# Optimization experiments

Measured on AMD Instinct MI355X. Metric: run time of the kernel, lower is better.

Reference implementation:

```python
import jax, jax.numpy as jnp
import numpy as np

B, S, D, H, HD = 1, 4096, 1024, 16, 64
HALF = HD // 2


def setup_inputs() -> dict:
    key = jax.random.key(0)
    ks = jax.random.split(key, 8)
    std = 0.02
    x = jax.random.normal(ks[0], (B, S, D), dtype=jnp.float32)
    wq_w = jax.random.normal(ks[1], (D, D), dtype=jnp.float32) * std
    wk_w = jax.random.normal(ks[2], (D, D), dtype=jnp.float32) * std
    wv_w = jax.random.normal(ks[3], (D, D), dtype=jnp.float32) * std
    wo_w = jax.random.normal(ks[4], (D, D), dtype=jnp.float32) * std
    wq_b = jnp.zeros((D,), jnp.float32)
    wk_b = jnp.zeros((D,), jnp.float32)
    wv_b = jnp.zeros((D,), jnp.float32)
    wo_b = jnp.zeros((D,), jnp.float32)
    # LLaMA-style rotary frequencies: theta = 10000^{-2i/HD}
    inv_freq = 1.0 / (10000.0 ** (jnp.arange(0, HD, 2, dtype=jnp.float32) / HD))  # [HALF]
    t = jnp.arange(S, dtype=jnp.float32)
    angles = jnp.outer(t, inv_freq)  # [S, HALF]
    freqs_cos = jnp.cos(angles)
    freqs_sin = jnp.sin(angles)
    # causal additive mask (finite large-negative to stay grad-safe)
    mask = jnp.triu(jnp.full((S, S), -1e9, dtype=jnp.float32), k=1)[None, None]
    return {
        "x": x, "start_pos": 0, "freqs_cos": freqs_cos, "freqs_sin": freqs_sin,
        "mask": mask,
        "wq_w": wq_w, "wq_b": wq_b, "wk_w": wk_w, "wk_b": wk_b,
        "wv_w": wv_w, "wv_b": wv_b, "wo_w": wo_w, "wo_b": wo_b,
    }


def _apply_rope(t, cos, sin):
    # t: [B, S, H, HD]; cos/sin: [S, HALF]. Complex multiply on consecutive pairs.
    b, s, h, hd = t.shape
    t2 = t.reshape(b, s, h, hd // 2, 2)
    x0, x1 = t2[..., 0], t2[..., 1]
    c = cos[None, :, None, :]
    sn = sin[None, :, None, :]
    o0 = x0 * c - x1 * sn
    o1 = x0 * sn + x1 * c
    return jnp.stack([o0, o1], axis=-1).reshape(b, s, h, hd)


def reference(x, start_pos, freqs_cos, freqs_sin, mask,
              wq_w, wq_b, wk_w, wk_b, wv_w, wv_b, wo_w, wo_b):
    bsz, seqlen, dim = x.shape
    q = (x @ wq_w.T + wq_b).reshape(bsz, seqlen, H, HD)
    k = (x @ wk_w.T + wk_b).reshape(bsz, seqlen, H, HD)
    v = (x @ wv_w.T + wv_b).reshape(bsz, seqlen, H, HD)
    q = _apply_rope(q, freqs_cos, freqs_sin)
    k = _apply_rope(k, freqs_cos, freqs_sin)
    # [B, H, S, HD]
    q = q.transpose(0, 2, 1, 3)
    k = k.transpose(0, 2, 1, 3)
    v = v.transpose(0, 2, 1, 3)
    scores = jnp.einsum('bhqd,bhkd->bhqk', q, k) / jnp.sqrt(jnp.float32(HD))
    scores = scores + mask
    probs = jax.nn.softmax(scores.astype(jnp.float32), axis=-1).astype(q.dtype)
    out = jnp.einsum('bhqk,bhkd->bhqd', probs, v)  # [B, H, S, HD]
    out = out.transpose(0, 2, 1, 3).reshape(bsz, seqlen, dim)
    return out @ wo_w.T + wo_b
```

## Files before the change

kernel.cpp:

```cpp
#include <hip/hip_runtime.h>


#define S_LEN 4096
#define DIM   1024
#define NH    16
#define HD    64

typedef __attribute__((ext_vector_type(8))) short bf16x8;
typedef __attribute__((ext_vector_type(4))) float f32x4;

__device__ __forceinline__ unsigned short f2b(float f) {
  union { float f; unsigned int u; } v; v.f = f;
  unsigned int r = (v.u + 0x7fffu + ((v.u >> 16) & 1u)) >> 16;
  return (unsigned short)r;
}
__device__ __forceinline__ float b2f(unsigned short h) {
  union { unsigned int u; float f; } v; v.u = ((unsigned int)h) << 16;
  return v.f;
}
__device__ __forceinline__ unsigned int pk2t(float a, float b) {
  union { float f; unsigned int u; } x, y; x.f = a; y.f = b;
  return (x.u >> 16) | (y.u & 0xffff0000u);
}
__device__ __forceinline__ void gload16(const void* g, void* l) {
  __builtin_amdgcn_global_load_lds(
      (const __attribute__((address_space(1))) unsigned int*)g,
      (__attribute__((address_space(3))) unsigned int*)l, 16, 0, 0);
}
__device__ __forceinline__ f32x4 fzero4() { f32x4 z = {0.f, 0.f, 0.f, 0.f}; return z; }

__global__ void cvt_all(const float* __restrict__ x, const float* __restrict__ wq,
                        const float* __restrict__ wk, const float* __restrict__ wv,
                        const float* __restrict__ wo, const float* __restrict__ qb,
                        const float* __restrict__ kb, const float* __restrict__ vbs,
                        const float* __restrict__ ob, unsigned short* __restrict__ xb,
                        unsigned short* __restrict__ wqkvb, unsigned short* __restrict__ wobb,
                        float* __restrict__ biasq, float* __restrict__ biaso) {
  int i = blockIdx.x * 256 + threadIdx.x;
  if (i < 2097152) {
    const float* src; unsigned short* dst; int off;
    if (i < 1048576)      { src = x;  dst = xb;              off = i; }
    else if (i < 1310720) { src = wq; dst = wqkvb;           off = i - 1048576; }
    else if (i < 1572864) { src = wk; dst = wqkvb + 1048576; off = i - 1310720; }
    else if (i < 1835008) { src = wv; dst = wqkvb + 2097152; off = i - 1572864; }
    else                  { src = wo; dst = wobb;            off = i - 1835008; }
    float4 v = ((const float4*)src)[off];
    unsigned int lo = (unsigned int)f2b(v.x) | ((unsigned int)f2b(v.y) << 16);
    unsigned int hi = (unsigned int)f2b(v.z) | ((unsigned int)f2b(v.w) << 16);
    ((uint2*)dst)[off] = make_uint2(lo, hi);
  } else if (i < 2097152 + 1024) {
    int j = i - 2097152;
    if (j < 256)      ((float4*)biasq)[j]              = ((const float4*)qb)[j];
    else if (j < 512) ((float4*)(biasq + 1024))[j-256] = ((const float4*)kb)[j-256];
    else if (j < 768) ((float4*)(biasq + 2048))[j-512] = ((const float4*)vbs)[j-512];
    else              ((float4*)biaso)[j-768]          = ((const float4*)ob)[j-768];
  }
}

__global__ __launch_bounds__(256) void gemm_qkv(
    const unsigned short* __restrict__ A, const unsigned short* __restrict__ B,
    const float* __restrict__ bias, unsigned short* __restrict__ dq,
    unsigned short* __restrict__ dk, unsigned short* __restrict__ vtout,
    const float* __restrict__ fc, const float* __restrict__ fs, int K) {
  __shared__ alignas(16) unsigned short sA[2][128 * 32];
  __shared__ alignas(16) unsigned short sB[2][128 * 32];
  const int tid = threadIdx.x;
  const int lane = tid & 63, wave = tid >> 6;
  const int ln = lane & 15, quad = lane >> 4;
  const int bm = blockIdx.x * 128, bn = blockIdx.y * 128;
  const int wr = (wave >> 1) * 64, wc = (wave & 1) * 64;

  f32x4 acc[4][4];
#pragma unroll
  for (int i = 0; i < 4; ++i)
#pragma unroll
    for (int j = 0; j < 4; ++j) acc[i][j] = fzero4();

#pragma unroll
  for (int i = 0; i < 2; ++i) {
    int o = (i * 256 + tid) * 16;
    int e = o >> 1;
    int row = e >> 5, col = e & 31;
    gload16(A + (size_t)(bm + row) * K + col, (char*)sA[0] + o);
    gload16(B + (size_t)(bn + row) * K + col, (char*)sB[0] + o);
  }

  int buf = 0;
  for (int k0 = 0; k0 < K; k0 += 32, buf ^= 1) {
    __syncthreads();
    if (k0 + 32 < K) {
#pragma unroll
      for (int i = 0; i < 2; ++i) {
        int o = (i * 256 + tid) * 16;
        int e = o >> 1;
        int row = e >> 5, col = e & 31;
        gload16(A + (size_t)(bm + row) * K + k0 + 32 + col, (char*)sA[buf ^ 1] + o);
        gload16(B + (size_t)(bn + row) * K + k0 + 32 + col, (char*)sB[buf ^ 1] + o);
      }
    }
    bf16x8 af[4], bfr[4];
#pragma unroll
    for (int i = 0; i < 4; ++i) {
      af[i]  = *(const bf16x8*)&sA[buf][(wr + i * 16 + ln) * 32 + quad * 8];
      bfr[i] = *(const bf16x8*)&sB[buf][(wc + i * 16 + ln) * 32 + quad * 8];
    }
#pragma unroll
    for (int i = 0; i < 4; ++i)
#pragma unroll
      for (int j = 0; j < 4; ++j)
        acc[i][j] = __builtin_amdgcn_mfma_f32_16x16x32_bf16(af[i], bfr[j], acc[i][j], 0, 0, 0);
  }

  const int bufi = bn >> 10;
  const int hq = ((bn & 1023) + wc) >> 6;
  if (bufi < 2) {
    unsigned short* const base = bufi == 0 ? dq : dk;
    const float qsc = bufi == 0 ? 0.180336880f : 1.0f;
#pragma unroll
    for (int i = 0; i < 4; ++i)
#pragma unroll
      for (int j = 0; j < 4; ++j) {
        int n = bn + wc + j * 16 + ln;
        float bi = bias[n];
        int hd = j * 16 + ln;
        int pi = hd >> 1;
        bool evn = (ln & 1) == 0;
#pragma unroll
        for (int r = 0; r < 4; ++r) {
          int m = bm + wr + i * 16 + quad * 4 + r;
          float val = acc[i][j][r] + bi;
          float par = __shfl_xor(val, 1);
          float c = fc[m * 32 + pi], sn = fs[m * 32 + pi];
          float o = evn ? (val * c - par * sn) : (par * sn + val * c);
          base[((size_t)(hq * S_LEN + m)) * HD + hd] = f2b(o * qsc);
        }
      }
  } else {
    __syncthreads();
    unsigned short* scr =
        (wave < 2 ? (unsigned short*)sA : (unsigned short*)sB) + (wave & 1) * 4096;
#pragma unroll
    for (int i = 0; i < 4; ++i)
#pragma unroll
      for (int j = 0; j < 4; ++j) {
        int n = bn + wc + j * 16 + ln;
        float bi = bias[n];
        int hd = j * 16 + ln;
#pragma unroll
        for (int r = 0; r < 4; ++r) {
          int sl = i * 16 + quad * 4 + r;
          int byte = hd * 128 + ((((sl >> 3) ^ (hd & 7)) << 4)) + (sl & 7) * 2;
          *(unsigned short*)((char*)scr + byte) = f2b(acc[i][j][r] + bi);
        }
      }
#pragma unroll
    for (int pass = 0; pass < 4; ++pass) {
      int row = pass * 16 + ln;
      uint4 d0 = *(uint4*)((char*)scr + row * 128 + (((quad * 2) ^ (row & 7)) << 4));
      uint4 d1 = *(uint4*)((char*)scr + row * 128 + (((quad * 2 + 1) ^ (row & 7)) << 4));
      uint4* dst = (uint4*)(vtout + ((size_t)(hq * HD + row)) * S_LEN + bm + wr + quad * 16);
      dst[0] = d0;
      dst[1] = d1;
    }
  }
}

__global__ __launch_bounds__(256) void gemm_out(
    const unsigned short* __restrict__ A, const unsigned short* __restrict__ B,
    const float* __restrict__ bias, float* __restrict__ outF, int N, int K) {
  __shared__ alignas(16) unsigned short sA[2][128 * 32];
  __shared__ alignas(16) unsigned short sB[2][64 * 32];
  const int tid = threadIdx.x;
  const int lane = tid & 63, wave = tid >> 6;
  const int ln = lane & 15, quad = lane >> 4;
  const int bm = blockIdx.x * 128, bn = blockIdx.y * 64;
  const int wr = (wave >> 1) * 64, wc = (wave & 1) * 32;

  f32x4 acc[4][2];
#pragma unroll
  for (int i = 0; i < 4; ++i)
#pragma unroll
    for (int j = 0; j < 2; ++j) acc[i][j] = fzero4();

  {
#pragma unroll
    for (int i = 0; i < 2; ++i) {
      int o = (i * 256 + tid) * 16;
      int e = o >> 1;
      int row = e >> 5, col = e & 31;
      gload16(A + (size_t)(bm + row) * K + col, (char*)sA[0] + o);
    }
    int o = tid * 16;
    int e = o >> 1;
    int row = e >> 5, col = e & 31;
    gload16(B + (size_t)(bn + row) * K + col, (char*)sB[0] + o);
  }

  int buf = 0;
  for (int k0 = 0; k0 < K; k0 += 32, buf ^= 1) {
    __syncthreads();
    if (k0 + 32 < K) {
#pragma unroll
      for (int i = 0; i < 2; ++i) {
        int o = (i * 256 + tid) * 16;
        int e = o >> 1;
        int row = e >> 5, col = e & 31;
        gload16(A + (size_t)(bm + row) * K + k0 + 32 + col, (char*)sA[buf ^ 1] + o);
      }
      int o = tid * 16;
      int e = o >> 1;
      int row = e >> 5, col = e & 31;
      gload16(B + (size_t)(bn + row) * K + k0 + 32 + col, (char*)sB[buf ^ 1] + o);
    }
    bf16x8 af[4], bfr[2];
#pragma unroll
    for (int i = 0; i < 4; ++i)
      af[i] = *(const bf16x8*)&sA[buf][(wr + i * 16 + ln) * 32 + quad * 8];
#pragma unroll
    for (int j = 0; j < 2; ++j)
      bfr[j] = *(const bf16x8*)&sB[buf][(wc + j * 16 + ln) * 32 + quad * 8];
#pragma unroll
    for (int i = 0; i < 4; ++i)
#pragma unroll
      for (int j = 0; j < 2; ++j)
        acc[i][j] = __builtin_amdgcn_mfma_f32_16x16x32_bf16(af[i], bfr[j], acc[i][j], 0, 0, 0);
  }

#pragma unroll
  for (int i = 0; i < 4; ++i)
#pragma unroll
    for (int j = 0; j < 2; ++j) {
      int n = bn + wc + j * 16 + ln;
      float bi = bias[n];
#pragma unroll
      for (int r = 0; r < 4; ++r) {
        int m = bm + wr + i * 16 + quad * 4 + r;
        outF[(size_t)m * N + n] = acc[i][j][r] + bi;
      }
    }
}

__device__ __forceinline__ bf16x8 lds_swz(const unsigned short* s, int row, int chunk) {
  int byte = row * 128 + ((chunk ^ (row & 7)) << 4);
  return *(const bf16x8*)((const char*)s + byte);
}

__global__ __launch_bounds__(512, 4) void flash_kernel(
    const unsigned short* __restrict__ qg, const unsigned short* __restrict__ kg,
    const unsigned short* __restrict__ vtg, unsigned short* __restrict__ attn) {
  __shared__ alignas(16) unsigned short sK[2][2][64 * 64];
  __shared__ alignas(16) unsigned short sV[2][2][64 * 64];

  const int tid = threadIdx.x;
  const int lane = tid & 63, wave = tid >> 6;
  const int w = wave & 3, grp = wave >> 2;
  const int ln = lane & 15, quad = lane >> 4;
  const int c = blockIdx.x;
  const int h = c & 15;
  const int qt = 63 - (c >> 4);
  const int qrow = qt * 64 + w * 16;

  const unsigned short* qh = qg + (size_t)h * (S_LEN * HD);
  const unsigned short* kh = kg + (size_t)h * (S_LEN * HD);
  const unsigned short* vh = vtg + (size_t)h * (HD * S_LEN);

  bf16x8 qf[2];
  qf[0] = *(const bf16x8*)(qh + (size_t)(qrow + ln) * HD + quad * 8);
  qf[1] = *(const bf16x8*)(qh + (size_t)(qrow + ln) * HD + 32 + quad * 8);

  f32x4 o_acc[4];
  f32x4 l_acc = fzero4();
#pragma unroll
  for (int t = 0; t < 4; ++t) o_acc[t] = fzero4();
  bf16x8 ones;
#pragma unroll
  for (int j = 0; j < 8; ++j) ones[j] = (short)0x3F80;

  const int nst = (qt + 2) >> 1;
  const int srow = tid >> 3, sch = tid & 7;
  const int kswz = (sch ^ (srow & 7)) << 3;

  gload16(kh + (size_t)srow * HD + kswz, (char*)sK[0][0] + tid * 16);
  gload16(kh + (size_t)(64 + srow) * HD + kswz, (char*)sK[0][1] + tid * 16);
  gload16(vh + (size_t)srow * S_LEN + kswz, (char*)sV[0][0] + tid * 16);
  gload16(vh + (size_t)srow * S_LEN + 64 + kswz, (char*)sV[0][1] + tid * 16);

  int buf = 0;
  for (int s = 0; s < nst; ++s, buf ^= 1) {
    __syncthreads();
    if (s + 1 < nst) {
      const int kvE = (2 * s + 2) * 64, kvO = kvE + 64;
      gload16(kh + (size_t)(kvE + srow) * HD + kswz, (char*)sK[buf ^ 1][0] + tid * 16);
      gload16(kh + (size_t)(kvO + srow) * HD + kswz, (char*)sK[buf ^ 1][1] + tid * 16);
      gload16(vh + (size_t)srow * S_LEN + kvE + kswz, (char*)sV[buf ^ 1][0] + tid * 16);
      gload16(vh + (size_t)srow * S_LEN + kvO + kswz, (char*)sV[buf ^ 1][1] + tid * 16);
    }
    const int kt = 2 * s + grp;
    if (kt > qt) continue;
    const int kv0 = kt * 64;
    const unsigned short* kp = sK[buf][grp];
    const unsigned short* vp = sV[buf][grp];

    f32x4 sc[4];
#pragma unroll
    for (int t = 0; t < 4; ++t) sc[t] = fzero4();
#pragma unroll
    for (int t = 0; t < 4; ++t) {
      bf16x8 kb0 = lds_swz(kp, t * 16 + ln, quad);
      bf16x8 kb1 = lds_swz(kp, t * 16 + ln, 4 + quad);
      sc[t] = __builtin_amdgcn_mfma_f32_16x16x32_bf16(kb0, qf[0], sc[t], 0, 0, 0);
      sc[t] = __builtin_amdgcn_mfma_f32_16x16x32_bf16(kb1, qf[1], sc[t], 0, 0, 0);
    }

    float e[4][4];
    if (kt == qt) {
#pragma unroll
      for (int t = 0; t < 4; ++t)
#pragma unroll
        for (int r = 0; r < 4; ++r) {
          int kvl = 16 * t + quad * 4 + r;
          e[t][r] = (kvl <= w * 16 + ln) ? __builtin_amdgcn_exp2f(sc[t][r]) : 0.0f;
        }
    } else {
#pragma unroll
      for (int t = 0; t < 4; ++t)
#pragma unroll
        for (int r = 0; r < 4; ++r) e[t][r] = __builtin_amdgcn_exp2f(sc[t][r]);
    }

    unsigned int x0 = pk2t(e[0][0], e[0][1]), x1 = pk2t(e[0][2], e[0][3]);
    unsigned int y0 = pk2t(e[1][0], e[1][1]), y1 = pk2t(e[1][2], e[1][3]);
    unsigned int z0 = pk2t(e[2][0], e[2][1]), z1 = pk2t(e[2][2], e[2][3]);
    unsigned int w0 = pk2t(e[3][0], e[3][1]), w1 = pk2t(e[3][2], e[3][3]);
    auto a32 = __builtin_amdgcn_permlane32_swap(x0, y0, false, false);
    auto a16 = __builtin_amdgcn_permlane16_swap(a32[0], a32[1], false, false);
    auto b32 = __builtin_amdgcn_permlane32_swap(x1, y1, false, false);
    auto b16 = __builtin_amdgcn_permlane16_swap(b32[0], b32[1], false, false);
    auto c32 = __builtin_amdgcn_permlane32_swap(z0, w0, false, false);
    auto c16 = __builtin_amdgcn_permlane16_swap(c32[0], c32[1], false, false);
    auto d32 = __builtin_amdgcn_permlane32_swap(z1, w1, false, false);
    auto d16 = __builtin_amdgcn_permlane16_swap(d32[0], d32[1], false, false);
    union { uint4 u; bf16x8 b; } pa0u, pa1u;
    pa0u.u = make_uint4(a16[0], b16[0], a16[1], b16[1]);
    pa1u.u = make_uint4(c16[0], d16[0], c16[1], d16[1]);
    const bf16x8 pa0 = pa0u.b, pa1 = pa1u.b;

    l_acc = __builtin_amdgcn_mfma_f32_16x16x32_bf16(pa0, ones, l_acc, 0, 0, 0);
    l_acc = __builtin_amdgcn_mfma_f32_16x16x32_bf16(pa1, ones, l_acc, 0, 0, 0);

#pragma unroll
    for (int t = 0; t < 4; ++t) {
      bf16x8 vb0 = lds_swz(vp, t * 16 + ln, quad);
      bf16x8 vb1 = lds_swz(vp, t * 16 + ln, 4 + quad);
      o_acc[t] = __builtin_amdgcn_mfma_f32_16x16x32_bf16(pa0, vb0, o_acc[t], 0, 0, 0);
      o_acc[t] = __builtin_amdgcn_mfma_f32_16x16x32_bf16(pa1, vb1, o_acc[t], 0, 0, 0);
    }
  }

  __syncthreads();
  float* mrg = (float*)sK;
  const int mi = (w * 64 + lane) * 20;
  if (grp == 1) {
    *(f32x4*)&mrg[mi +  0] = o_acc[0];
    *(f32x4*)&mrg[mi +  4] = o_acc[1];
    *(f32x4*)&mrg[mi +  8] = o_acc[2];
    *(f32x4*)&mrg[mi + 12] = o_acc[3];
    *(f32x4*)&mrg[mi + 16] = l_acc;
  }
  __syncthreads();
  if (grp == 0) {
    o_acc[0] += *(const f32x4*)&mrg[mi + 0];
    o_acc[1] += *(const f32x4*)&mrg[mi + 4];
    o_acc[2] += *(const f32x4*)&mrg[mi + 8];
    o_acc[3] += *(const f32x4*)&mrg[mi + 12];
    l_acc += *(const f32x4*)&mrg[mi + 16];
    float inv[4];
#pragma unroll
    for (int r = 0; r < 4; ++r) inv[r] = 1.0f / l_acc[r];
#pragma unroll
    for (int t = 0; t < 4; ++t)
#pragma unroll
      for (int r = 0; r < 4; ++r) {
        int row = qrow + quad * 4 + r;
        attn[(size_t)row * DIM + h * HD + t * 16 + ln] = f2b(o_acc[t][r] * inv[r]);
      }
  }
}

extern "C" void kernel_launch(void* const* d_in, const int* in_sizes, int n_in,
                              void* d_out, int out_size, void* d_ws, size_t ws_size,
                              hipStream_t stream) {
  const float* x    = (const float*)d_in[0];
  const float* fc   = (const float*)d_in[2];
  const float* fs   = (const float*)d_in[3];
  const float* wqw  = (const float*)d_in[5];
  const float* wqb  = (const float*)d_in[6];
  const float* wkw  = (const float*)d_in[7];
  const float* wkb  = (const float*)d_in[8];
  const float* wvw  = (const float*)d_in[9];
  const float* wvb  = (const float*)d_in[10];
  const float* wow  = (const float*)d_in[11];
  const float* wobf = (const float*)d_in[12];
  float* out = (float*)d_out;

  char* ws = (char*)d_ws;
  const size_t MB = (size_t)1 << 20;
  unsigned short* xb    = (unsigned short*)(ws + 0);
  unsigned short* wqkvb = (unsigned short*)(ws + 8 * MB);
  unsigned short* wobb  = (unsigned short*)(ws + 16 * MB);
  float* biasq = (float*)(ws + 18 * MB);
  float* biaso = (float*)(ws + 18 * MB + 65536);
  unsigned short* qb_ = (unsigned short*)(ws + 19 * MB);
  unsigned short* kb_ = (unsigned short*)(ws + 27 * MB);
  unsigned short* vt  = (unsigned short*)(ws + 35 * MB);
  unsigned short* attn = (unsigned short*)(ws + 0);

  cvt_all<<<8196, 256, 0, stream>>>(x, wqw, wkw, wvw, wow, wqb, wkb, wvb, wobf,
                                    xb, wqkvb, wobb, biasq, biaso);
  gemm_qkv<<<dim3(32, 24), 256, 0, stream>>>(xb, wqkvb, biasq, qb_, kb_, vt, fc, fs, 1024);
  flash_kernel<<<1024, 512, 0, stream>>>(qb_, kb_, vt, attn);
  gemm_out<<<dim3(32, 16), 256, 0, stream>>>(attn, wobb, biaso, out, 1024, 1024);
}
```

Baseline: 249.8 us.

## Enlarge QKV GEMM tiles to 256x256x64 with swizzled LDS and 512 threads

Reworks the QKV projection GEMM so each block computes a 256x256 output tile with 8 waves and a K-step of 64. LDS staging now uses an XOR swizzle to avoid bank conflicts, and the V-transpose epilogue is adapted to the wider tiles. The aim is more data reuse per LDS load and fewer global loads per output. In exchange the grid shrinks to 192 blocks, which may underfill the 256 CUs, and the larger accumulators raise register and LDS pressure (128KB of LDS).

```diff
diff --git a/kernel.cpp b/kernel.cpp
--- a/kernel.cpp
+++ b/kernel.cpp
@@ -28,6 +28,11 @@
       (__attribute__((address_space(3))) unsigned int*)l, 16, 0, 0);
 }
 __device__ __forceinline__ f32x4 fzero4() { f32x4 z = {0.f, 0.f, 0.f, 0.f}; return z; }
+
+__device__ __forceinline__ bf16x8 lds_swz(const unsigned short* s, int row, int chunk) {
+  int byte = row * 128 + ((chunk ^ (row & 7)) << 4);
+  return *(const bf16x8*)((const char*)s + byte);
+}
 
 __global__ void cvt_all(const float* __restrict__ x, const float* __restrict__ wq,
                         const float* __restrict__ wk, const float* __restrict__ wv,
@@ -57,58 +62,62 @@
   }
 }
 
-__global__ __launch_bounds__(256) void gemm_qkv(
+__global__ __launch_bounds__(512, 2) void gemm_qkv(
     const unsigned short* __restrict__ A, const unsigned short* __restrict__ B,
     const float* __restrict__ bias, unsigned short* __restrict__ dq,
     unsigned short* __restrict__ dk, unsigned short* __restrict__ vtout,
     const float* __restrict__ fc, const float* __restrict__ fs, int K) {
-  __shared__ alignas(16) unsigned short sA[2][128 * 32];
-  __shared__ alignas(16) unsigned short sB[2][128 * 32];
+  __shared__ alignas(16) unsigned short sA[2][256 * 64];
+  __shared__ alignas(16) unsigned short sB[2][256 * 64];
   const int tid = threadIdx.x;
   const int lane = tid & 63, wave = tid >> 6;
   const int ln = lane & 15, quad = lane >> 4;
-  const int bm = blockIdx.x * 128, bn = blockIdx.y * 128;
-  const int wr = (wave >> 1) * 64, wc = (wave & 1) * 64;
-
-  f32x4 acc[4][4];
-#pragma unroll
-  for (int i = 0; i < 4; ++i)
+  const int bm = blockIdx.x * 256, bn = blockIdx.y * 256;
+  const int wr = (wave >> 2) * 128, wc = (wave & 3) * 64;
+
+  f32x4 acc[8][4];
+#pragma unroll
+  for (int i = 0; i < 8; ++i)
 #pragma unroll
     for (int j = 0; j < 4; ++j) acc[i][j] = fzero4();
 
 #pragma unroll
-  for (int i = 0; i < 2; ++i) {
-    int o = (i * 256 + tid) * 16;
-    int e = o >> 1;
-    int row = e >> 5, col = e & 31;
-    gload16(A + (size_t)(bm + row) * K + col, (char*)sA[0] + o);
-    gload16(B + (size_t)(bn + row) * K + col, (char*)sB[0] + o);
+  for (int i = 0; i < 4; ++i) {
+    int o = (i * 512 + tid) * 8;
+    int row = o >> 6, c = (o >> 3) & 7;
+    int col = ((c ^ (row & 7)) << 3);
+    gload16(A + (size_t)(bm + row) * K + col, (char*)sA[0] + o * 2);
+    gload16(B + (size_t)(bn + row) * K + col, (char*)sB[0] + o * 2);
   }
 
   int buf = 0;
-  for (int k0 = 0; k0 < K; k0 += 32, buf ^= 1) {
+  for (int k0 = 0; k0 < K; k0 += 64, buf ^= 1) {
     __syncthreads();
-    if (k0 + 32 < K) {
-#pragma unroll
-      for (int i = 0; i < 2; ++i) {
-        int o = (i * 256 + tid) * 16;
-        int e = o >> 1;
-        int row = e >> 5, col = e & 31;
-        gload16(A + (size_t)(bm + row) * K + k0 + 32 + col, (char*)sA[buf ^ 1] + o);
-        gload16(B + (size_t)(bn + row) * K + k0 + 32 + col, (char*)sB[buf ^ 1] + o);
-      }
-    }
-    bf16x8 af[4], bfr[4];
-#pragma unroll
-    for (int i = 0; i < 4; ++i) {
-      af[i]  = *(const bf16x8*)&sA[buf][(wr + i * 16 + ln) * 32 + quad * 8];
-      bfr[i] = *(const bf16x8*)&sB[buf][(wc + i * 16 + ln) * 32 + quad * 8];
-    }
-#pragma unroll
-    for (int i = 0; i < 4; ++i)
+    if (k0 + 64 < K) {
+#pragma unroll
+      for (int i = 0; i < 4; ++i) {
+        int o = (i * 512 + tid) * 8;
+        int row = o >> 6, c = (o >> 3) & 7;
+        int col = k0 + 64 + ((c ^ (row & 7)) << 3);
+        gload16(A + (size_t)(bm + row) * K + col, (char*)sA[buf ^ 1] + o * 2);
+        gload16(B + (size_t)(bn + row) * K + col, (char*)sB[buf ^ 1] + o * 2);
+      }
+    }
+#pragma unroll
+    for (int ks = 0; ks < 2; ++ks) {
+      bf16x8 af[8], bfr[4];
+#pragma unroll
+      for (int i = 0; i < 8; ++i)
+        af[i] = lds_swz(sA[buf], wr + i * 16 + ln, ks * 4 + quad);
 #pragma unroll
       for (int j = 0; j < 4; ++j)
-        acc[i][j] = __builtin_amdgcn_mfma_f32_16x16x32_bf16(af[i], bfr[j], acc[i][j], 0, 0, 0);
+        bfr[j] = lds_swz(sB[buf], wc + j * 16 + ln, ks * 4 + quad);
+#pragma unroll
+      for (int i = 0; i < 8; ++i)
+#pragma unroll
+        for (int j = 0; j < 4; ++j)
+          acc[i][j] = __builtin_amdgcn_mfma_f32_16x16x32_bf16(af[i], bfr[j], acc[i][j], 0, 0, 0);
+    }
   }
 
   const int bufi = bn >> 10;
@@ -117,7 +126,7 @@
     unsigned short* const base = bufi == 0 ? dq : dk;
     const float qsc = bufi == 0 ? 0.180336880f : 1.0f;
 #pragma unroll
-    for (int i = 0; i < 4; ++i)
+    for (int i = 0; i < 8; ++i)
 #pragma unroll
       for (int j = 0; j < 4; ++j) {
         int n = bn + wc + j * 16 + ln;
@@ -138,9 +147,9 @@
   } else {
     __syncthreads();
     unsigned short* scr =
-        (wave < 2 ? (unsigned short*)sA : (unsigned short*)sB) + (wave & 1) * 4096;
-#pragma unroll
-    for (int i = 0; i < 4; ++i)
+        (wave < 4 ? (unsigned short*)sA : (unsigned short*)sB) + (wave & 3) * 8192;
+#pragma unroll
+    for (int i = 0; i < 8; ++i)
 #pragma unroll
       for (int j = 0; j < 4; ++j) {
         int n = bn + wc + j * 16 + ln;
@@ -149,18 +158,22 @@
 #pragma unroll
         for (int r = 0; r < 4; ++r) {
           int sl = i * 16 + quad * 4 + r;
-          int byte = hd * 128 + ((((sl >> 3) ^ (hd & 7)) << 4)) + (sl & 7) * 2;
+          int byte = hd * 256 + ((((sl >> 3) ^ (hd & 7)) << 4)) + (sl & 7) * 2;
           *(unsigned short*)((char*)scr + byte) = f2b(acc[i][j][r] + bi);
         }
       }
 #pragma unroll
     for (int pass = 0; pass < 4; ++pass) {
       int row = pass * 16 + ln;
-      uint4 d0 = *(uint4*)((char*)scr + row * 128 + (((quad * 2) ^ (row & 7)) << 4));
-      uint4 d1 = *(uint4*)((char*)scr + row * 128 + (((quad * 2 + 1) ^ (row & 7)) << 4));
-      uint4* dst = (uint4*)(vtout + ((size_t)(hq * HD + row)) * S_LEN + bm + wr + quad * 16);
-      dst[0] = d0;
-      dst[1] = d1;
+      uint4 d[4];
+#pragma unroll
+      for (int j = 0; j < 4; ++j) {
+        int c = quad * 4 + j;
+        d[j] = *(uint4*)((char*)scr + row * 256 + ((c ^ (row & 7)) << 4));
+      }
+      uint4* dst = (uint4*)(vtout + ((size_t)(hq * HD + row)) * S_LEN + bm + wr + quad * 32);
+#pragma unroll
+      for (int j = 0; j < 4; ++j) dst[j] = d[j];
     }
   }
 }
@@ -240,11 +253,6 @@
     }
 }
 
-__device__ __forceinline__ bf16x8 lds_swz(const unsigned short* s, int row, int chunk) {
-  int byte = row * 128 + ((chunk ^ (row & 7)) << 4);
-  return *(const bf16x8*)((const char*)s + byte);
-}
-
 __global__ __launch_bounds__(512, 4) void flash_kernel(
     const unsigned short* __restrict__ qg, const unsigned short* __restrict__ kg,
     const unsigned short* __restrict__ vtg, unsigned short* __restrict__ attn) {
@@ -297,7 +305,6 @@
     }
     const int kt = 2 * s + grp;
     if (kt > qt) continue;
-    const int kv0 = kt * 64;
     const unsigned short* kp = sK[buf][grp];
     const unsigned short* vp = sV[buf][grp];
 
@@ -417,7 +424,7 @@
 
   cvt_all<<<8196, 256, 0, stream>>>(x, wqw, wkw, wvw, wow, wqb, wkb, wvb, wobf,
                                     xb, wqkvb, wobb, biasq, biaso);
-  gemm_qkv<<<dim3(32, 24), 256, 0, stream>>>(xb, wqkvb, biasq, qb_, kb_, vt, fc, fs, 1024);
+  gemm_qkv<<<dim3(16, 12), 512, 0, stream>>>(xb, wqkvb, biasq, qb_, kb_, vt, fc, fs, 1024);
   flash_kernel<<<1024, 512, 0, stream>>>(qb_, kb_, vt, attn);
   gemm_out<<<dim3(32, 16), 256, 0, stream>>>(attn, wobb, biaso, out, 1024, 1024);
 }
```

Result: no change. 248.9 us (-0.4%).
